# Optimization experiments

Hardware: AMD Instinct MI355X
Metric: run time of the kernel (lower is better)

Reference implementation:

```python
import jax, jax.numpy as jnp
import numpy as np

B, C, H, W = 4, 256, 56, 56
N = H * W  # 3136 tokens


def setup_inputs() -> dict:
    key = jax.random.key(0)
    ks = jax.random.split(key, 12)
    f = lambda k, s: jax.random.normal(k, s, dtype=jnp.float32)
    return {
        "feat0": f(ks[0], (B, 1, C, H, W)),
        "feat1": f(ks[1], (B, 1, C, H, W)),
        "feat2": f(ks[2], (B, 1, C, H, W)),
        "feat3": f(ks[3], (B, 1, C, H, W)),
        "hist0": jax.random.uniform(ks[4], (B, N), dtype=jnp.float32),
        "hist1": jax.random.uniform(ks[5], (B, N), dtype=jnp.float32),
        "hist2": jax.random.uniform(ks[6], (B, N), dtype=jnp.float32),
        "mask": f(ks[7], (N, N)),
        "Wv": f(ks[8], (C, C)) * 0.02,   # v_linear weight (torch layout [out,in])
        "bv": jnp.zeros((C,), jnp.float32),
        "Wl": f(ks[9], (C, 2 * C)) * 0.02,  # low_channel weight
        "bl": jnp.zeros((C,), jnp.float32),
    }


def _tokens(x5d):
    # [b,1,c,h,w] -> [b, n, c]
    b = x5d.shape[0]
    return x5d.reshape(b, C, N).transpose(0, 2, 1)


def _to5d(tok):
    # [b,n,c] -> [b,1,c,h,w]
    b = tok.shape[0]
    return tok.transpose(0, 2, 1).reshape(b, 1, C, H, W)


def reference(feat0, feat1, feat2, feat3, hist0, hist1, hist2, mask, Wv, bv, Wl, bl):
    scale = 1.0 / jnp.sqrt(jnp.float32(C))

    def stage(q_tok, feat5d):
        f = _tokens(feat5d)                                   # [b,n,c]
        corr = jnp.einsum('bnc,bmc->bnm', q_tok, f) * scale   # [b,n,n]
        p = jax.nn.softmax(corr + mask[None], axis=-1)        # masked softmax
        v = f @ Wv.T + bv                                     # v_linear
        motion = jnp.einsum('bnm,bmc->bnc', p, v)             # attention
        refined = motion + f                                  # residual
        out = jnp.concatenate([refined, f], axis=-1) @ Wl.T + bl  # low_channel
        return refined, out

    # histograms (hist0..hist2) are consumed by the original module but its
    # histogram_mask is dead code; they do not affect the math.
    q = _tokens(feat0)
    refined, out1 = stage(q, feat1)
    refined, out2 = stage(refined, feat2)
    refined, out3 = stage(refined, feat3)

    return jnp.concatenate(
        [feat0, _to5d(out1), _to5d(out2), _to5d(out3)], axis=1
    )  # [b, 4, c, h, w]
```

## Files before the change

kernel.cpp:

```cpp
#include <hip/hip_runtime.h>
#include <hip/hip_bf16.h>

#define B_   4
#define C_   256
#define N_   3136
#define QT_  196
#define NKV_ 98
#define CH_  5

typedef __attribute__((ext_vector_type(8)))  short bf16x8;
typedef __attribute__((ext_vector_type(4)))  float f32x4;
typedef __attribute__((ext_vector_type(16))) float f32x16;

#define LOG2E  1.4426950408889634f
#define SCALE2 (LOG2E / 16.0f)
#define FMAX_  20.0f

__device__ __forceinline__ unsigned short bfbits(float f) {
  __hip_bfloat16 h = __float2bfloat16(f);
  return *(unsigned short*)&h;
}
__device__ __forceinline__ unsigned cvtpk(float lo, float hi) {
  unsigned r;
  asm("v_cvt_pk_bf16_f32 %0, %1, %2" : "=v"(r) : "v"(lo), "v"(hi));
  return r;
}

__device__ __forceinline__ void gld16(const void* g, void* l) {
  __builtin_amdgcn_global_load_lds(
      (const __attribute__((address_space(1))) unsigned int*)g,
      (__attribute__((address_space(3))) unsigned int*)l, 16, 0, 0);
}

__device__ __forceinline__ int vperm(int n) {
  int k = n & 31;
  return (n & ~31) | (k & 16) | (((k >> 2) & 1) << 3) | (k & 3) | (((k >> 3) & 1) << 2);
}

__global__ __launch_bounds__(256) void transpose4_kernel(
    const float* __restrict__ f0, const float* __restrict__ f1,
    const float* __restrict__ f2, const float* __restrict__ f3,
    __hip_bfloat16* __restrict__ d0, __hip_bfloat16* __restrict__ d1,
    __hip_bfloat16* __restrict__ d2, __hip_bfloat16* __restrict__ d3,
    float* __restrict__ out) {
  __shared__ float tile[32][33];
  const int z  = blockIdx.z;
  const int fi = z >> 2;
  const int b  = z & 3;
  const float* src = (fi == 0) ? f0 : (fi == 1) ? f1 : (fi == 2) ? f2 : f3;
  __hip_bfloat16* dst = (fi == 0) ? d0 : (fi == 1) ? d1 : (fi == 2) ? d2 : d3;
  const int n0 = blockIdx.x * 32;
  const int c0 = blockIdx.y * 32;
  const int tx = threadIdx.x & 31;
  const int ty = threadIdx.x >> 5;
  const float* s = src + (size_t)b * C_ * N_;
  float* ob = out + (size_t)b * 4 * C_ * N_;
#pragma unroll
  for (int i = 0; i < 4; ++i) {
    int c = c0 + ty + i * 8;
    float v = s[(size_t)c * N_ + n0 + tx];
    tile[ty + i * 8][tx] = v;
    if (fi == 0) ob[(size_t)c * N_ + n0 + tx] = v;
  }
  __syncthreads();
  __hip_bfloat16* d = dst + (size_t)b * N_ * C_;
#pragma unroll
  for (int i = 0; i < 4; ++i) {
    int n = n0 + ty + i * 8;
    d[(size_t)n * C_ + c0 + tx] = __float2bfloat16(tile[tx][ty + i * 8]);
  }
}

__global__ __launch_bounds__(256) void cvt_all_kernel(
    const float* __restrict__ Wv, const float* __restrict__ Wl,
    const float* __restrict__ mask,
    __hip_bfloat16* __restrict__ Wvb, __hip_bfloat16* __restrict__ Wlb,
    __hip_bfloat16* __restrict__ maskb) {
  int i = blockIdx.x * 256 + threadIdx.x;
  if (i < 24576) {
    const float* src; __hip_bfloat16* dst; int off;
    if (i < 8192) { src = Wv; dst = Wvb; off = i; }
    else          { src = Wl; dst = Wlb; off = i - 8192; }
    const float4* s4 = (const float4*)src;
    float4 a = s4[2 * off], b = s4[2 * off + 1];
    union { unsigned short u[8]; bf16x8 v; } p;
    p.u[0]=bfbits(a.x); p.u[1]=bfbits(a.y); p.u[2]=bfbits(a.z); p.u[3]=bfbits(a.w);
    p.u[4]=bfbits(b.x); p.u[5]=bfbits(b.y); p.u[6]=bfbits(b.z); p.u[7]=bfbits(b.w);
    *(bf16x8*)(dst + 8 * off) = p.v;
    return;
  }
  int j = i - 24576;
  if (j >= NKV_ * NKV_ * 32 * 2) return;
  const int hi  = j & 1;
  const int cl  = (j >> 1) & 31;
  const int rem = j >> 6;
  const int kt  = rem % NKV_;
  const int qu  = rem / NKV_;
  const int q   = qu * 32 + cl;
  const float* s = mask + (size_t)q * N_ + kt * 32 + 4 * hi;
  float4 a0 = *(const float4*)(s);
  float4 a1 = *(const float4*)(s + 8);
  float4 a2 = *(const float4*)(s + 16);
  float4 a3 = *(const float4*)(s + 24);
  union { unsigned short u[16]; bf16x8 v[2]; } p;
  p.u[0]=bfbits(a0.x*LOG2E); p.u[1]=bfbits(a0.y*LOG2E); p.u[2]=bfbits(a0.z*LOG2E); p.u[3]=bfbits(a0.w*LOG2E);
  p.u[4]=bfbits(a1.x*LOG2E); p.u[5]=bfbits(a1.y*LOG2E); p.u[6]=bfbits(a1.z*LOG2E); p.u[7]=bfbits(a1.w*LOG2E);
  p.u[8]=bfbits(a2.x*LOG2E); p.u[9]=bfbits(a2.y*LOG2E); p.u[10]=bfbits(a2.z*LOG2E); p.u[11]=bfbits(a2.w*LOG2E);
  p.u[12]=bfbits(a3.x*LOG2E); p.u[13]=bfbits(a3.y*LOG2E); p.u[14]=bfbits(a3.z*LOG2E); p.u[15]=bfbits(a3.w*LOG2E);
  __hip_bfloat16* d = maskb + ((size_t)rem * 32 + cl) * 32 + hi * 16;
  *(bf16x8*)(d)     = p.v[0];
  *(bf16x8*)(d + 8) = p.v[1];
}

__global__ __launch_bounds__(256) void v_linear_kernel(
    const __hip_bfloat16* __restrict__ f1, const __hip_bfloat16* __restrict__ f2,
    const __hip_bfloat16* __restrict__ f3,
    const __hip_bfloat16* __restrict__ Wv, const float* __restrict__ bv,
    __hip_bfloat16* __restrict__ vT0, __hip_bfloat16* __restrict__ vT1,
    __hip_bfloat16* __restrict__ vT2)
{
  const int s    = blockIdx.z;
  const int b    = blockIdx.y;
  const int nblk = blockIdx.x;
  const __hip_bfloat16* fb = (s == 0) ? f1 : (s == 1) ? f2 : f3;
  __hip_bfloat16* vT = (s == 0) ? vT0 : (s == 1) ? vT1 : vT2;
  const int wave = threadIdx.x >> 6;
  const int lane = threadIdx.x & 63;
  const int qt = lane & 15, g = lane >> 4;
  const int n0 = nblk * 64;
  const __hip_bfloat16* fbb = fb + (size_t)b * N_ * C_;
  const int c0 = wave * 64;
  f32x4 acc[4][4];
#pragma unroll
  for (int u = 0; u < 4; ++u)
#pragma unroll
    for (int j = 0; j < 4; ++j) acc[u][j] = (f32x4){0.f, 0.f, 0.f, 0.f};
#pragma unroll
  for (int kk = 0; kk < 8; ++kk) {
    int ko = kk * 32 + g * 8;
    bf16x8 bb[4];
#pragma unroll
    for (int j = 0; j < 4; ++j)
      bb[j] = *(const bf16x8*)(fbb + (size_t)(n0 + j * 16 + qt) * C_ + ko);
#pragma unroll
    for (int u = 0; u < 4; ++u) {
      bf16x8 a = *(const bf16x8*)(Wv + (size_t)(c0 + u * 16 + qt) * C_ + ko);
#pragma unroll
      for (int j = 0; j < 4; ++j)
        acc[u][j] = __builtin_amdgcn_mfma_f32_16x16x32_bf16(a, bb[j], acc[u][j], 0, 0, 0);
    }
  }
  __hip_bfloat16* outp = vT + (size_t)b * C_ * N_;
#pragma unroll
  for (int u = 0; u < 4; ++u)
#pragma unroll
    for (int j = 0; j < 4; ++j)
#pragma unroll
      for (int r = 0; r < 4; ++r) {
        int c = c0 + u * 16 + 4 * g + r;
        int n = vperm(n0 + j * 16 + qt);
        outp[(size_t)c * N_ + n] = __float2bfloat16(acc[u][j][r] + bv[c]);
      }
}

__global__ __launch_bounds__(256, 2) void attn_kernel(
    const __hip_bfloat16* __restrict__ qb,
    const __hip_bfloat16* __restrict__ kb,
    const __hip_bfloat16* __restrict__ vT,
    const __hip_bfloat16* __restrict__ mb,
    unsigned* __restrict__ pOb,
    float* __restrict__ pML)
{
  __shared__ __hip_bfloat16 Kl[2][32 * 256];
  __shared__ __hip_bfloat16 Vl[2][32 * 256];

  const int bid   = blockIdx.x;
  const int grp   = bid % 20;
  const int qblk  = bid / 20;
  const int b     = grp / CH_;
  const int chunk = grp % CH_;
  const int wave  = threadIdx.x >> 6;
  const int lane  = threadIdx.x & 63;
  const int cl = lane & 31, hi = lane >> 5;
  const int qunit = qblk * 4 + wave;
  const bool valid = qunit < 98;
  const int qu = valid ? qunit : 97;
  const int q0row = qu * 32 + cl;
  const int t0 = (chunk * NKV_) / CH_;
  const int t1 = ((chunk + 1) * NKV_) / CH_;
  const int nt = t1 - t0;
  const int tid = threadIdx.x;

  const __hip_bfloat16* qbb = qb + (size_t)b * N_ * C_;
  const char* kbbc = (const char*)(kb + (size_t)b * N_ * C_);
  const char* vbbc = (const char*)(vT + (size_t)b * C_ * N_);
  const char* mbase = (const char*)mb + (size_t)qu * (NKV_ * 2048) + cl * 64 + hi * 32;

  bf16x8 qa[16];
#pragma unroll
  for (int ks = 0; ks < 16; ++ks)
    qa[ks] = *(const bf16x8*)(qbb + (size_t)q0row * C_ + ks * 16 + 8 * hi);

  f32x16 o[8];
#pragma unroll
  for (int ct = 0; ct < 8; ++ct)
#pragma unroll
    for (int r = 0; r < 16; ++r) o[ct][r] = 0.f;
  float lsum = 0.f;

  auto STAGE = [&](int buf, int t) {
    const char* ks0 = kbbc + (size_t)t * 32 * 512;
#pragma unroll
    for (int i = 0; i < 4; ++i) {
      int g2 = tid + i * 256;
      int ks = g2 >> 6, h2 = (g2 >> 5) & 1, key = g2 & 31;
      gld16(ks0 + key * 512 + ks * 32 + h2 * 16, (char*)&Kl[buf][0] + g2 * 16);
    }
    const char* vs0 = vbbc + (size_t)t * 64;
#pragma unroll
    for (int i = 0; i < 4; ++i) {
      int g2 = tid + i * 256;
      int st = g2 >> 9, h2 = (g2 >> 8) & 1, c = g2 & 255;
      gld16(vs0 + (size_t)c * (N_ * 2) + st * 32 + h2 * 16, (char*)&Vl[buf][0] + g2 * 16);
    }
  };

  union { uint4 v[2]; unsigned w[8]; } mm;
  auto MLOAD = [&](int t) {
    mm.v[0] = *(const uint4*)(mbase + (size_t)t * 2048);
    mm.v[1] = *(const uint4*)(mbase + (size_t)t * 2048 + 16);
  };

  STAGE(0, t0);
  MLOAD(t0);

  const int kread = hi * 512 + cl * 16;
  const int vread = hi * 4096 + cl * 16;

  for (int tt = 0; tt < nt; ++tt) {
    const int buf = tt & 1;
    const bool nl = (tt + 1 < nt);
    if (nl) STAGE(buf ^ 1, t0 + tt + 1);
    if (nl) asm volatile("s_waitcnt vmcnt(10)" ::: "memory");
    else    asm volatile("s_waitcnt vmcnt(2)"  ::: "memory");
    __builtin_amdgcn_s_barrier();

    f32x16 sA, sB;
#pragma unroll
    for (int r = 0; r < 16; ++r) { sA[r] = 0.f; sB[r] = 0.f; }
    if (valid) {
      const char* Kb = (const char*)&Kl[buf][0] + kread;
      __builtin_amdgcn_s_setprio(1);
#pragma unroll
      for (int ks = 0; ks < 8; ++ks) {
        bf16x8 kf0 = *(const bf16x8*)(Kb + ks * 2048);
        bf16x8 kf1 = *(const bf16x8*)(Kb + ks * 2048 + 1024);
        sA = __builtin_amdgcn_mfma_f32_32x32x16_bf16(kf0, qa[2 * ks],     sA, 0, 0, 0);
        sB = __builtin_amdgcn_mfma_f32_32x32x16_bf16(kf1, qa[2 * ks + 1], sB, 0, 0, 0);
      }
      __builtin_amdgcn_s_setprio(0);
    }

    if (valid) {
      float p[16];
#pragma unroll
      for (int j = 0; j < 16; ++j) {
        unsigned wo = mm.w[j >> 1];
        float mf = __uint_as_float((j & 1) ? (wo & 0xffff0000u) : (wo << 16));
        p[j] = exp2f(fmaf(sA[j] + sB[j], SCALE2, mf) - FMAX_);
      }
      lsum += ((p[0]+p[1])+(p[2]+p[3])) + ((p[4]+p[5])+(p[6]+p[7]))
            + ((p[8]+p[9])+(p[10]+p[11])) + ((p[12]+p[13])+(p[14]+p[15]));

      union { unsigned u[4]; bf16x8 v8; } A0, A1;
#pragma unroll
      for (int k = 0; k < 4; ++k) A0.u[k] = cvtpk(p[2 * k], p[2 * k + 1]);
#pragma unroll
      for (int k = 0; k < 4; ++k) A1.u[k] = cvtpk(p[8 + 2 * k], p[9 + 2 * k]);

      const char* Vb = (const char*)&Vl[buf][0] + vread;
      __builtin_amdgcn_s_setprio(1);
#pragma unroll
      for (int ct = 0; ct < 8; ++ct) {
        bf16x8 vf0 = *(const bf16x8*)(Vb + ct * 512);
        o[ct] = __builtin_amdgcn_mfma_f32_32x32x16_bf16(A0.v8, vf0, o[ct], 0, 0, 0);
        bf16x8 vf1 = *(const bf16x8*)(Vb + 8192 + ct * 512);
        o[ct] = __builtin_amdgcn_mfma_f32_32x32x16_bf16(A1.v8, vf1, o[ct], 0, 0, 0);
      }
      __builtin_amdgcn_s_setprio(0);
    }
    if (nl) MLOAD(t0 + tt + 1);
    __builtin_amdgcn_s_barrier();
  }

  if (valid) {
    float lt = lsum + __shfl_xor(lsum, 32);
#pragma unroll
    for (int r = 0; r < 16; ++r) {
      int q = (r & 3) + 8 * (r >> 2) + 4 * hi;
      int qt16 = qu * 2 + (q >> 4);
      int row = q & 15;
      size_t ob = ((((size_t)b * QT_ + qt16) * CH_ + chunk) * 2048) + row * 128 + cl;
#pragma unroll
      for (int pp = 0; pp < 4; ++pp)
        pOb[ob + pp * 32] = cvtpk(o[2 * pp][r], o[2 * pp + 1][r]);
    }
    if (lane < 32) {
      int qt16 = qu * 2 + (cl >> 4);
      int row = cl & 15;
      float* pml = pML + (((size_t)b * QT_ + qt16) * CH_ + chunk) * 32;
      pml[row] = FMAX_;
      pml[16 + row] = lt;
    }
  }
}

__global__ __launch_bounds__(256) void combine_kernel(
    const unsigned* __restrict__ pOb, const float* __restrict__ pML,
    const __hip_bfloat16* __restrict__ fb,
    __hip_bfloat16* __restrict__ ref)
{
  __shared__ float sml[CH_ * 32];
  const int b = blockIdx.y;
  const int qtile = blockIdx.x;
  const int tid = threadIdx.x;
  const float* pml = pML + ((size_t)b * QT_ + qtile) * (CH_ * 32);
  if (tid < CH_ * 32) sml[tid] = pml[tid];
  __syncthreads();

  const int w  = tid & 127;
  const int r0 = (tid >> 7) * 8;
  const int ch_lo = 64 * (w >> 5) + (w & 31);
  const int ch_hi = ch_lo + 32;

  float wgt[CH_][8];
#pragma unroll
  for (int r = 0; r < 8; ++r) {
    int row = r0 + r;
    float M = sml[row];
#pragma unroll
    for (int ch = 1; ch < CH_; ++ch) M = fmaxf(M, sml[ch * 32 + row]);
    float L = 0.f;
#pragma unroll
    for (int ch = 0; ch < CH_; ++ch) {
      float wv = exp2f(sml[ch * 32 + row] - M);
      wgt[ch][r] = wv;
      L += wv * sml[ch * 32 + 16 + row];
    }
    float iL = 1.f / L;
#pragma unroll
    for (int ch = 0; ch < CH_; ++ch) wgt[ch][r] *= iL;
  }

  float acc_lo[8], acc_hi[8];
#pragma unroll
  for (int r = 0; r < 8; ++r) { acc_lo[r] = 0.f; acc_hi[r] = 0.f; }
  const unsigned* base = pOb + ((size_t)b * QT_ + qtile) * (CH_ * 2048) + r0 * 128 + w;
#pragma unroll
  for (int ch = 0; ch < CH_; ++ch) {
    const unsigned* p = base + ch * 2048;
#pragma unroll
    for (int r = 0; r < 8; ++r) {
      unsigned u = p[r * 128];
      acc_lo[r] += wgt[ch][r] * __uint_as_float(u << 16);
      acc_hi[r] += wgt[ch][r] * __uint_as_float(u & 0xffff0000u);
    }
  }

  const __hip_bfloat16* f = fb + ((size_t)b * N_ + qtile * 16 + r0) * C_;
  __hip_bfloat16* rf = ref + ((size_t)b * N_ + qtile * 16 + r0) * C_;
#pragma unroll
  for (int r = 0; r < 8; ++r) {
    rf[r * C_ + ch_lo] = __float2bfloat16(acc_lo[r] + __bfloat162float(f[r * C_ + ch_lo]));
    rf[r * C_ + ch_hi] = __float2bfloat16(acc_hi[r] + __bfloat162float(f[r * C_ + ch_hi]));
  }
}

__global__ __launch_bounds__(256) void out_linear_kernel(
    const __hip_bfloat16* __restrict__ refb,
    const __hip_bfloat16* __restrict__ fb,
    const __hip_bfloat16* __restrict__ Wl,
    const float* __restrict__ bl,
    float* __restrict__ out)
{
  const int b    = blockIdx.z;
  const int cblk = blockIdx.y;
  const int nblk = blockIdx.x;
  const int wave = threadIdx.x >> 6;
  const int lane = threadIdx.x & 63;
  const int qt = lane & 15, g = lane >> 4;
  const int c0 = cblk * 128 + wave * 32;
  const int n0 = nblk * 32;
  const __hip_bfloat16* rb  = refb + (size_t)b * N_ * C_;
  const __hip_bfloat16* fbb = fb  + (size_t)b * N_ * C_;
  f32x4 acc[2][2];
#pragma unroll
  for (int u = 0; u < 2; ++u)
#pragma unroll
    for (int j = 0; j < 2; ++j) acc[u][j] = (f32x4){0.f, 0.f, 0.f, 0.f};
#pragma unroll
  for (int kk = 0; kk < 16; ++kk) {
    int ko = kk * 32 + g * 8;
    const __hip_bfloat16* src = (kk < 8) ? rb : fbb;
    int ko2 = ko & 255;
    bf16x8 bb0 = *(const bf16x8*)(src + (size_t)(n0 + qt) * C_ + ko2);
    bf16x8 bb1 = *(const bf16x8*)(src + (size_t)(n0 + 16 + qt) * C_ + ko2);
#pragma unroll
    for (int u = 0; u < 2; ++u) {
      bf16x8 a = *(const bf16x8*)(Wl + (size_t)(c0 + u * 16 + qt) * 512 + ko);
      acc[u][0] = __builtin_amdgcn_mfma_f32_16x16x32_bf16(a, bb0, acc[u][0], 0, 0, 0);
      acc[u][1] = __builtin_amdgcn_mfma_f32_16x16x32_bf16(a, bb1, acc[u][1], 0, 0, 0);
    }
  }
  float* ob = out + (size_t)b * 4 * C_ * N_;
#pragma unroll
  for (int u = 0; u < 2; ++u)
#pragma unroll
    for (int j = 0; j < 2; ++j)
#pragma unroll
      for (int r = 0; r < 4; ++r) {
        int c = c0 + u * 16 + 4 * g + r;
        int n = n0 + j * 16 + qt;
        ob[(size_t)c * N_ + n] = acc[u][j][r] + bl[c];
      }
}

extern "C" void kernel_launch(void* const* d_in, const int* in_sizes, int n_in,
                              void* d_out, int out_size, void* d_ws, size_t ws_size,
                              hipStream_t stream) {
  (void)in_sizes; (void)n_in; (void)out_size; (void)ws_size;
  const float* feat0 = (const float*)d_in[0];
  const float* feat1 = (const float*)d_in[1];
  const float* feat2 = (const float*)d_in[2];
  const float* feat3 = (const float*)d_in[3];
  const float* mask  = (const float*)d_in[7];
  const float* Wv    = (const float*)d_in[8];
  const float* bv    = (const float*)d_in[9];
  const float* Wl    = (const float*)d_in[10];
  const float* bl    = (const float*)d_in[11];
  float* out = (float*)d_out;

  const size_t TOKB = (size_t)B_ * N_ * C_ * 2;
  char* w = (char*)d_ws;
  __hip_bfloat16* q0   = (__hip_bfloat16*)(w);
  __hip_bfloat16* f1   = (__hip_bfloat16*)(w + TOKB);
  __hip_bfloat16* f2   = (__hip_bfloat16*)(w + 2 * TOKB);
  __hip_bfloat16* f3   = (__hip_bfloat16*)(w + 3 * TOKB);
  __hip_bfloat16* vT0  = (__hip_bfloat16*)(w + 4 * TOKB);
  __hip_bfloat16* vT1  = (__hip_bfloat16*)(w + 5 * TOKB);
  __hip_bfloat16* vT2  = (__hip_bfloat16*)(w + 6 * TOKB);
  char* w2 = w + 7 * TOKB;
  __hip_bfloat16* Wv_bf = (__hip_bfloat16*)(w2);
  __hip_bfloat16* Wl_bf = (__hip_bfloat16*)(w2 + 131072);
  __hip_bfloat16* maskb = (__hip_bfloat16*)(w2 + 393216);
  unsigned* pOb         = (unsigned*)(w2 + 393216 + 19668992);
  float* pML            = (float*)(w2 + 393216 + 19668992 + (size_t)B_ * QT_ * CH_ * 4096 * 2);

  dim3 tb(256);
  transpose4_kernel<<<dim3(98, 8, 16), tb, 0, stream>>>(feat0, feat1, feat2, feat3,
                                                        q0, f1, f2, f3, out);
  cvt_all_kernel<<<dim3((24576 + NKV_ * NKV_ * 64 + 255) / 256), tb, 0, stream>>>(
      Wv, Wl, mask, Wv_bf, Wl_bf, maskb);
  v_linear_kernel<<<dim3(49, 4, 3), tb, 0, stream>>>(f1, f2, f3, Wv_bf, bv,
                                                     vT0, vT1, vT2);

  const __hip_bfloat16* fs[3] = {f1, f2, f3};
  const __hip_bfloat16* vTs[3] = {vT0, vT1, vT2};
  __hip_bfloat16* refs[3] = {vT0, vT1, vT0};
  const __hip_bfloat16* q = q0;
  for (int s = 0; s < 3; ++s) {
    attn_kernel<<<dim3(500), tb, 0, stream>>>(q, fs[s], vTs[s], maskb, pOb, pML);
    combine_kernel<<<dim3(196, 4), tb, 0, stream>>>(pOb, pML, fs[s], refs[s]);
    out_linear_kernel<<<dim3(98, 2, 4), tb, 0, stream>>>(refs[s], fs[s], Wl_bf, bl,
                                                         out + (size_t)(s + 1) * C_ * N_);
    q = refs[s];
  }
}
```

Before: 383.8 us.

## Pre-swizzle weights into MFMA fragment order and use single QK accumulator

The weight conversion kernel now writes Wv and Wl in bf16 in a fragment-major layout, so each lane's A operand for the 16x16x32 MFMA is one contiguous 16-byte load and a wave's load is fully coalesced, replacing strided row loads. Separately, the attention QK^T loop now uses a single accumulator chain of 16 MFMAs instead of two interleaved chains of 8. That saves registers and the final add but serialises dependent MFMAs, which may expose latency.

```diff
diff --git a/kernel.cpp b/kernel.cpp
--- a/kernel.cpp
+++ b/kernel.cpp
@@ -78,15 +78,24 @@
     __hip_bfloat16* __restrict__ maskb) {
   int i = blockIdx.x * 256 + threadIdx.x;
   if (i < 24576) {
-    const float* src; __hip_bfloat16* dst; int off;
-    if (i < 8192) { src = Wv; dst = Wvb; off = i; }
-    else          { src = Wl; dst = Wlb; off = i - 8192; }
+    const float* src; __hip_bfloat16* dstp; int off, dst8;
+    if (i < 8192) {
+      off = i; src = Wv; dstp = Wvb;
+      int row = off >> 5, c8 = off & 31;
+      int ct = row >> 4, qt = row & 15, kk = c8 >> 2, g = c8 & 3;
+      dst8 = (ct * 8 + kk) * 64 + g * 16 + qt;
+    } else {
+      off = i - 8192; src = Wl; dstp = Wlb;
+      int row = off >> 6, c8 = off & 63;
+      int ct = row >> 4, qt = row & 15, kk = c8 >> 2, g = c8 & 3;
+      dst8 = (ct * 16 + kk) * 64 + g * 16 + qt;
+    }
     const float4* s4 = (const float4*)src;
     float4 a = s4[2 * off], b = s4[2 * off + 1];
     union { unsigned short u[8]; bf16x8 v; } p;
     p.u[0]=bfbits(a.x); p.u[1]=bfbits(a.y); p.u[2]=bfbits(a.z); p.u[3]=bfbits(a.w);
     p.u[4]=bfbits(b.x); p.u[5]=bfbits(b.y); p.u[6]=bfbits(b.z); p.u[7]=bfbits(b.w);
-    *(bf16x8*)(dst + 8 * off) = p.v;
+    *(bf16x8*)(dstp + 8 * dst8) = p.v;
     return;
   }
   int j = i - 24576;
@@ -115,7 +124,8 @@
 __global__ __launch_bounds__(256) void v_linear_kernel(
     const __hip_bfloat16* __restrict__ f1, const __hip_bfloat16* __restrict__ f2,
     const __hip_bfloat16* __restrict__ f3,
-    const __hip_bfloat16* __restrict__ Wv, const float* __restrict__ bv,
+    const __hip_bfloat16* __restrict__ Wv,
+    const float* __restrict__ bv,
     __hip_bfloat16* __restrict__ vT0, __hip_bfloat16* __restrict__ vT1,
     __hip_bfloat16* __restrict__ vT2)
 {
@@ -144,7 +154,7 @@
       bb[j] = *(const bf16x8*)(fbb + (size_t)(n0 + j * 16 + qt) * C_ + ko);
 #pragma unroll
     for (int u = 0; u < 4; ++u) {
-      bf16x8 a = *(const bf16x8*)(Wv + (size_t)(c0 + u * 16 + qt) * C_ + ko);
+      bf16x8 a = *(const bf16x8*)(Wv + (size_t)(((wave * 4 + u) * 8 + kk) * 64 + lane) * 8);
 #pragma unroll
       for (int j = 0; j < 4; ++j)
         acc[u][j] = __builtin_amdgcn_mfma_f32_16x16x32_bf16(a, bb[j], acc[u][j], 0, 0, 0);
@@ -245,18 +255,16 @@
     else    asm volatile("s_waitcnt vmcnt(2)"  ::: "memory");
     __builtin_amdgcn_s_barrier();
 
-    f32x16 sA, sB;
-#pragma unroll
-    for (int r = 0; r < 16; ++r) { sA[r] = 0.f; sB[r] = 0.f; }
+    f32x16 s;
+#pragma unroll
+    for (int r = 0; r < 16; ++r) s[r] = 0.f;
     if (valid) {
       const char* Kb = (const char*)&Kl[buf][0] + kread;
       __builtin_amdgcn_s_setprio(1);
 #pragma unroll
-      for (int ks = 0; ks < 8; ++ks) {
-        bf16x8 kf0 = *(const bf16x8*)(Kb + ks * 2048);
-        bf16x8 kf1 = *(const bf16x8*)(Kb + ks * 2048 + 1024);
-        sA = __builtin_amdgcn_mfma_f32_32x32x16_bf16(kf0, qa[2 * ks],     sA, 0, 0, 0);
-        sB = __builtin_amdgcn_mfma_f32_32x32x16_bf16(kf1, qa[2 * ks + 1], sB, 0, 0, 0);
+      for (int ks = 0; ks < 16; ++ks) {
+        bf16x8 kf = *(const bf16x8*)(Kb + ks * 1024);
+        s = __builtin_amdgcn_mfma_f32_32x32x16_bf16(kf, qa[ks], s, 0, 0, 0);
       }
       __builtin_amdgcn_s_setprio(0);
     }
@@ -267,7 +275,7 @@
       for (int j = 0; j < 16; ++j) {
         unsigned wo = mm.w[j >> 1];
         float mf = __uint_as_float((j & 1) ? (wo & 0xffff0000u) : (wo << 16));
-        p[j] = exp2f(fmaf(sA[j] + sB[j], SCALE2, mf) - FMAX_);
+        p[j] = exp2f(fmaf(s[j], SCALE2, mf) - FMAX_);
       }
       lsum += ((p[0]+p[1])+(p[2]+p[3])) + ((p[4]+p[5])+(p[6]+p[7]))
             + ((p[8]+p[9])+(p[10]+p[11])) + ((p[12]+p[13])+(p[14]+p[15]));
@@ -400,14 +408,14 @@
     for (int j = 0; j < 2; ++j) acc[u][j] = (f32x4){0.f, 0.f, 0.f, 0.f};
 #pragma unroll
   for (int kk = 0; kk < 16; ++kk) {
-    int ko = kk * 32 + g * 8;
+    int ko2 = (kk * 32 + g * 8) & 255;
     const __hip_bfloat16* src = (kk < 8) ? rb : fbb;
-    int ko2 = ko & 255;
     bf16x8 bb0 = *(const bf16x8*)(src + (size_t)(n0 + qt) * C_ + ko2);
     bf16x8 bb1 = *(const bf16x8*)(src + (size_t)(n0 + 16 + qt) * C_ + ko2);
 #pragma unroll
     for (int u = 0; u < 2; ++u) {
-      bf16x8 a = *(const bf16x8*)(Wl + (size_t)(c0 + u * 16 + qt) * 512 + ko);
+      int ct = cblk * 8 + wave * 2 + u;
+      bf16x8 a = *(const bf16x8*)(Wl + (size_t)((ct * 16 + kk) * 64 + lane) * 8);
       acc[u][0] = __builtin_amdgcn_mfma_f32_16x16x32_bf16(a, bb0, acc[u][0], 0, 0, 0);
       acc[u][1] = __builtin_amdgcn_mfma_f32_16x16x32_bf16(a, bb1, acc[u][1], 0, 0, 0);
     }
```

New measurement: 329.3 us. -14.2%, faster.
